# Performance work log

Measured on AMD Instinct MI355X. Metric: run time of the kernel, lower is better.

## Reference

```python
import jax, jax.numpy as jnp
import numpy as np

H = W = 224
NUM_COLS = 1024          # static padded ring width (>= max pixels in any radial ring, ~703)
SHUFFLE_FRACTION = 0.5
BATCH = 128

def _build_maps():
    centre = (H // 2, W // 2)
    Y, X = np.ogrid[:H, :W]
    dist = np.round(np.sqrt((X - centre[0]) ** 2 + (Y - centre[1]) ** 2)).astype(np.int32)
    num_rows = int(dist[0, 0]) + 1
    ax2 = np.zeros_like(dist)
    for d in range(num_rows):
        m = dist == d
        ax2[m] = np.arange(m.sum(), dtype=np.int32)  # row-major order within each ring
    return dist, ax2, num_rows

_DIST_NP, _AX2_NP, NUM_ROWS = _build_maps()
DIST_FLAT = jnp.asarray(_DIST_NP.reshape(-1))  # (H*W,) radial bin of each pixel
AX2_FLAT = jnp.asarray(_AX2_NP.reshape(-1))    # (H*W,) index within its ring

def _process_one(img, mrand, prand):
    # img: (H, W); mrand: (H, W); prand: (NUM_ROWS, NUM_COLS)
    sel = mrand < SHUFFLE_FRACTION
    masked = jnp.where(sel, img, jnp.nan)
    # scatter selected pixels into polar bins (pixel -> (dist, ax2) is a bijection)
    polar = jnp.full((NUM_ROWS, NUM_COLS), jnp.nan, dtype=img.dtype)
    polar = polar.at[DIST_FLAT, AX2_FLAT].set(masked.reshape(-1))
    # random per-row permutation of columns
    perm = jnp.argsort(prand, axis=1)
    shuf = jnp.take_along_axis(polar, perm, axis=1)
    # compact the non-NaN shuffled values (in column order) back into the
    # originally-occupied columns (in ascending order) -- same as the TF
    # argsort(dists)/boolean-mask scatter, expressed with static shapes.
    src_order = jnp.argsort(jnp.isnan(shuf), axis=1)    # stable: non-NaN cols first
    vals = jnp.take_along_axis(shuf, src_order, axis=1)
    dst_order = jnp.argsort(jnp.isnan(polar), axis=1)   # stable: occupied cols first
    rows = jnp.arange(NUM_ROWS)[:, None]
    reinserted = shuf.at[rows, dst_order].set(vals)
    # gather each pixel's (possibly shuffled) value and write back selected pixels
    new_vals = reinserted[DIST_FLAT, AX2_FLAT].reshape(H, W)
    return jnp.where(sel, new_vals, img)

def setup_inputs() -> dict:
    key = jax.random.key(0)
    k1, k2, k3 = jax.random.split(key, 3)
    images = jax.random.normal(k1, (BATCH, H, W, 1), dtype=jnp.float32)
    mask_rand = jax.random.uniform(k2, (BATCH, H, W), dtype=jnp.float32)
    perm_rand = jax.random.uniform(k3, (BATCH, NUM_ROWS, NUM_COLS), dtype=jnp.float32)
    return {"images": images, "mask_rand": mask_rand, "perm_rand": perm_rand}

def reference(images, mask_rand, perm_rand):
    out = jax.vmap(_process_one)(images[..., 0], mask_rand, perm_rand)
    return out[..., None]
```

## Files before the change

### kernel.cpp

```cpp
#include <hip/hip_runtime.h>

#define IMG_H 224
#define IMG_W 224
#define HW (IMG_H * IMG_W)
#define NUM_ROWS 159
#define NUM_COLS 1024
#define BATCH 128
#define OVF_CAP 4096
#define MAXC 12
#define NBUCK 512
#define NHWORDS (NBUCK / 2)

__device__ __forceinline__ int isqrt_i(int v) {
    int u = (int)sqrtf((float)v);
    while (u > 0 && u * u > v) --u;
    while ((u + 1) * (u + 1) <= v) ++u;
    return u;
}

__device__ __forceinline__ void lds_fence() {
    asm volatile("s_waitcnt lgkmcnt(0)" ::: "memory");
}

__global__ __launch_bounds__(256) void build_rings(int* __restrict__ ring_pix,
                                                   int* __restrict__ ring_cnt,
                                                   int* __restrict__ ovf_cnt) {
    const int d = blockIdx.x;
    const int tid = threadIdx.x;
    __shared__ int scnt[256];
    if (d == 0 && tid == 0) ovf_cnt[0] = 0;

    int cnt = 0;
    int x0l = 0, x1l = -1, x0r = 0, x1r = -1;
    if (tid < IMG_H) {
        const int dy = tid - 112;
        const int Araw = (d == 0) ? 0 : (d * d - d + 1);
        int A = Araw - dy * dy;
        if (A < 0) A = 0;
        const int B = d * d + d - dy * dy;
        if (B >= 0) {
            const int hi = isqrt_i(B);
            int lo = isqrt_i(A);
            if (lo * lo < A) ++lo;
            if (lo <= hi) {
                if (lo == 0) {
                    x0l = 112 - min(hi, 112);
                    x1l = 112 + min(hi, 111);
                } else {
                    x0l = 112 - min(hi, 112);
                    x1l = 112 - lo;
                    x0r = 112 + lo;
                    x1r = 112 + min(hi, 111);
                }
                cnt = max(0, x1l - x0l + 1) + max(0, x1r - x0r + 1);
            }
        }
    }
    scnt[tid] = cnt;
    __syncthreads();
    for (int off = 1; off < 256; off <<= 1) {
        const int mine = scnt[tid];
        const int add = (tid >= off) ? scnt[tid - off] : 0;
        __syncthreads();
        scnt[tid] = mine + add;
        __syncthreads();
    }
    if (tid < IMG_H && cnt > 0) {
        int j = d * NUM_COLS + (scnt[tid] - cnt);
        const int rowbase = tid * IMG_W;
        for (int x = x0l; x <= x1l; ++x) ring_pix[j++] = rowbase + x;
        for (int x = x0r; x <= x1r; ++x) ring_pix[j++] = rowbase + x;
    }
    if (tid == 255) ring_cnt[d] = scnt[255];
}

template <int CAP>
__device__ int gather_count_sort(
    int b, int d, int lane,
    const float* __restrict__ img, const float* __restrict__ mask,
    const float* __restrict__ prand, float* __restrict__ out,
    const int* __restrict__ ring_pix, int n,
    unsigned long long* __restrict__ srt, unsigned* __restrict__ hist,
    unsigned short* __restrict__ dstpix) {
    const float* imgb  = img  + (size_t)b * HW;
    const float* maskb = mask + (size_t)b * HW;
    const float* prb   = prand + ((size_t)b * NUM_ROWS + d) * NUM_COLS;
    float* outb = out + (size_t)b * HW;
    const unsigned long long ltmask = (1ull << lane) - 1ull;
    const int* rp = ring_pix + d * NUM_COLS;

#pragma unroll
    for (int t = 0; t < NHWORDS / 64; ++t) hist[t * 64 + lane] = 0;

    int p[MAXC];
    float v[MAXC], m[MAXC];
    unsigned kb[MAXC];
#pragma unroll
    for (int c = 0; c < MAXC; ++c) p[c] = rp[min(c * 64 + lane, n - 1)];
#pragma unroll
    for (int c = 0; c < MAXC; ++c) v[c] = imgb[p[c]];
#pragma unroll
    for (int c = 0; c < MAXC; ++c) m[c] = maskb[p[c]];
#pragma unroll
    for (int c = 0; c < MAXC; ++c)
        kb[c] = __float_as_uint(prb[min(c * 64 + lane, n - 1)]);

    lds_fence();

    int base = 0;
#pragma unroll
    for (int c = 0; c < MAXC; ++c) {
        const int i = c * 64 + lane;
        const bool active = (i < n);
        const bool sel = active && (m[c] < 0.5f);
        if (active && !sel) outb[p[c]] = v[c];
        const unsigned long long ball = __ballot(sel);
        if (sel) {
            const int j = base + __popcll(ball & ltmask);
            if (j < CAP) dstpix[j] = (unsigned short)p[c];
            const int bk = (int)(__uint_as_float(kb[c]) * (float)NBUCK);
            atomicAdd(&hist[bk >> 1], 1u << ((bk & 1) * 16));
        }
        base += __popcll(ball);
    }
    for (int c0 = MAXC * 64; c0 < n; c0 += 64) {
        const int i = c0 + lane;
        bool sel = false;
        int pp = 0;
        unsigned kk = 0;
        if (i < n) {
            pp = rp[i];
            const float vv = imgb[pp];
            kk = __float_as_uint(prb[i]);
            sel = (maskb[pp] < 0.5f);
            if (!sel) outb[pp] = vv;
        }
        const unsigned long long ball = __ballot(sel);
        if (sel) {
            const int j = base + __popcll(ball & ltmask);
            if (j < CAP) dstpix[j] = (unsigned short)pp;
            const int bk = (int)(__uint_as_float(kk) * (float)NBUCK);
            atomicAdd(&hist[bk >> 1], 1u << ((bk & 1) * 16));
        }
        base += __popcll(ball);
    }
    const int k = base;
    if (k > CAP) return k;

    lds_fence();

    constexpr int WPL = NHWORDS / 64;
    unsigned neww[WPL];
    unsigned run = 0;
#pragma unroll
    for (int t = 0; t < WPL; ++t) {
        const unsigned w = hist[lane * WPL + t];
        const unsigned c0 = w & 0xffffu;
        neww[t] = run | ((run + c0) << 16);
        run += c0 + (w >> 16);
    }
    const unsigned own = run;
#pragma unroll
    for (int off = 1; off < 64; off <<= 1) {
        const unsigned o = __shfl_up(run, off, 64);
        if (lane >= off) run += o;
    }
    const unsigned basex = run - own;
#pragma unroll
    for (int t = 0; t < WPL; ++t)
        hist[lane * WPL + t] = neww[t] + (basex | (basex << 16));

    lds_fence();

#pragma unroll
    for (int c = 0; c < MAXC; ++c) {
        const int i = c * 64 + lane;
        if (i < n && m[c] < 0.5f) {
            const int bk = (int)(__uint_as_float(kb[c]) * (float)NBUCK);
            const unsigned sh = (unsigned)((bk & 1) * 16);
            const unsigned old = atomicAdd(&hist[bk >> 1], 1u << sh);
            const int pos = (int)((old >> sh) & 0xffffu);
            srt[pos] = ((unsigned long long)kb[c] << 16) | (unsigned)p[c];
        }
    }
    for (int c0 = MAXC * 64; c0 < n; c0 += 64) {
        const int i = c0 + lane;
        if (i < n) {
            const int pp = rp[i];
            if (maskb[pp] < 0.5f) {
                const unsigned kk = __float_as_uint(prb[i]);
                const int bk = (int)(__uint_as_float(kk) * (float)NBUCK);
                const unsigned sh = (unsigned)((bk & 1) * 16);
                const unsigned old = atomicAdd(&hist[bk >> 1], 1u << sh);
                const int pos = (int)((old >> sh) & 0xffffu);
                srt[pos] = ((unsigned long long)kk << 16) | (unsigned)pp;
            }
        }
    }

    lds_fence();

    while (true) {
        bool sw = false;
        for (int i0 = 2 * lane; i0 + 1 < k; i0 += 128) {
            const unsigned long long a = srt[i0], bb = srt[i0 + 1];
            if (a > bb) { srt[i0] = bb; srt[i0 + 1] = a; sw = true; }
        }
        lds_fence();
        for (int i0 = 2 * lane + 1; i0 + 1 < k; i0 += 128) {
            const unsigned long long a = srt[i0], bb = srt[i0 + 1];
            if (a > bb) { srt[i0] = bb; srt[i0 + 1] = a; sw = true; }
        }
        lds_fence();
        if (__ballot(sw) == 0) break;
    }
    return k;
}

__device__ __forceinline__ void scatter_out(
    const unsigned long long* __restrict__ srt,
    const unsigned short* __restrict__ dstpix, int k, int lane,
    const float* __restrict__ imgb, float* __restrict__ outb) {
    const unsigned short* s16 = (const unsigned short*)srt;
    for (int j = lane; j < k; j += 64) {
        const int psrc = s16[4 * j];
        const int pdst = dstpix[j];
        outb[pdst] = imgb[psrc];
    }
}

__global__ __launch_bounds__(256) void radial_shuffle(
    const float* __restrict__ img, const float* __restrict__ mask,
    const float* __restrict__ prand, float* __restrict__ out,
    const int* __restrict__ ring_pix, const int* __restrict__ ring_cnt,
    int* __restrict__ ovf_cnt, int* __restrict__ ovf_list) {
    const int tid = threadIdx.x;
    const int wid = tid >> 6;
    const int lane = tid & 63;
    const int xcd = blockIdx.x & 7;
    const int g = (blockIdx.x >> 3) * 4 + wid;
    const int b = xcd * (BATCH / 8) + g / NUM_ROWS;
    const int d = g % NUM_ROWS;
    const int n = ring_cnt[d];

    __shared__ unsigned long long srt_s[4][512];
    __shared__ unsigned hist_s[4][NHWORDS];
    __shared__ unsigned short dp_s[4][512];

    const int k = gather_count_sort<512>(b, d, lane, img, mask, prand, out,
                                         ring_pix, n, srt_s[wid], hist_s[wid],
                                         dp_s[wid]);

    if (k > 512) {
        if (lane == 0) {
            const int idx = atomicAdd(ovf_cnt, 1);
            if (idx < OVF_CAP) ovf_list[idx] = b * NUM_ROWS + d;
        }
    } else if (k > 0) {
        scatter_out(srt_s[wid], dp_s[wid], k, lane, img + (size_t)b * HW,
                    out + (size_t)b * HW);
    }
}

__global__ __launch_bounds__(64) void overflow_sort(
    const float* __restrict__ img, const float* __restrict__ mask,
    const float* __restrict__ prand, float* __restrict__ out,
    const int* __restrict__ ring_pix, const int* __restrict__ ring_cnt,
    const int* __restrict__ ovf_cnt, const int* __restrict__ ovf_list) {
    __shared__ unsigned long long srt[1024];
    __shared__ unsigned hist[NHWORDS];
    __shared__ unsigned short dstpix[1024];
    const int m = min(*ovf_cnt, OVF_CAP);
    const int lane = threadIdx.x;
    for (int t = blockIdx.x; t < m; t += gridDim.x) {
        const int bd = ovf_list[t];
        const int b = bd / NUM_ROWS;
        const int d = bd % NUM_ROWS;
        const int k = gather_count_sort<1024>(b, d, lane, img, mask, prand,
                                              out, ring_pix, ring_cnt[d], srt,
                                              hist, dstpix);
        scatter_out(srt, dstpix, k, lane, img + (size_t)b * HW,
                    out + (size_t)b * HW);
        __syncthreads();
    }
}

extern "C" void kernel_launch(void* const* d_in, const int* in_sizes, int n_in,
                              void* d_out, int out_size, void* d_ws, size_t ws_size,
                              hipStream_t stream) {
    const float* img   = (const float*)d_in[0];
    const float* mask  = (const float*)d_in[1];
    const float* prand = (const float*)d_in[2];
    float* out = (float*)d_out;

    int* ring_pix = (int*)d_ws;
    int* ring_cnt = ring_pix + NUM_ROWS * NUM_COLS;
    int* ovf_cnt  = ring_cnt + NUM_ROWS;
    int* ovf_list = ovf_cnt + 1;

    hipLaunchKernelGGL(build_rings, dim3(NUM_ROWS), dim3(256), 0, stream,
                       ring_pix, ring_cnt, ovf_cnt);
    hipLaunchKernelGGL(radial_shuffle, dim3(BATCH * NUM_ROWS / 4), dim3(256), 0,
                       stream, img, mask, prand, out, ring_pix, ring_cnt,
                       ovf_cnt, ovf_list);
    hipLaunchKernelGGL(overflow_sort, dim3(32), dim3(64), 0, stream,
                       img, mask, prand, out, ring_pix, ring_cnt,
                       ovf_cnt, ovf_list);
}
```

Before: 231.7 us.

## Precompute selection bitmask with coalesced copy pass, replace odd-even sort with per-bucket insertion sort

Adds a coalesced float4 pre-pass that copies the image to the output and packs mask<0.5 into a per-pixel bitmask. The ring kernel then no longer does scattered reads of the mask or writes of unselected pixels. Ring pixel indices shrink to 16-bit, and image values are staged in LDS so only selected pixels are gathered. The odd-even transposition sort is replaced by per-bucket insertion sort over the bucket ranges, which relies on buckets being small. This costs an extra full-image read and write pass and an extra kernel launch.

```diff
diff --git a/kernel.cpp b/kernel.cpp
--- a/kernel.cpp
+++ b/kernel.cpp
@@ -3,6 +3,7 @@
 #define IMG_H 224
 #define IMG_W 224
 #define HW (IMG_H * IMG_W)
+#define HWB (HW / 8)
 #define NUM_ROWS 159
 #define NUM_COLS 1024
 #define BATCH 128
@@ -10,6 +11,7 @@
 #define MAXC 12
 #define NBUCK 512
 #define NHWORDS (NBUCK / 2)
+#define WPL (NHWORDS / 64)
 
 __device__ __forceinline__ int isqrt_i(int v) {
     int u = (int)sqrtf((float)v);
@@ -22,7 +24,7 @@
     asm volatile("s_waitcnt lgkmcnt(0)" ::: "memory");
 }
 
-__global__ __launch_bounds__(256) void build_rings(int* __restrict__ ring_pix,
+__global__ __launch_bounds__(256) void build_rings(unsigned short* __restrict__ ring_pix,
                                                    int* __restrict__ ring_cnt,
                                                    int* __restrict__ ovf_cnt) {
     const int d = blockIdx.x;
@@ -68,52 +70,89 @@
     if (tid < IMG_H && cnt > 0) {
         int j = d * NUM_COLS + (scnt[tid] - cnt);
         const int rowbase = tid * IMG_W;
-        for (int x = x0l; x <= x1l; ++x) ring_pix[j++] = rowbase + x;
-        for (int x = x0r; x <= x1r; ++x) ring_pix[j++] = rowbase + x;
+        for (int x = x0l; x <= x1l; ++x) ring_pix[j++] = (unsigned short)(rowbase + x);
+        for (int x = x0r; x <= x1r; ++x) ring_pix[j++] = (unsigned short)(rowbase + x);
     }
     if (tid == 255) ring_cnt[d] = scnt[255];
+}
+
+__global__ __launch_bounds__(256) void copy_sel(const float4* __restrict__ img4,
+                                                const float4* __restrict__ mask4,
+                                                float4* __restrict__ out4,
+                                                unsigned char* __restrict__ selb) {
+    const int t = blockIdx.x * 256 + threadIdx.x;
+    const float4 i0 = img4[2 * t];
+    const float4 i1 = img4[2 * t + 1];
+    const float4 m0 = mask4[2 * t];
+    const float4 m1 = mask4[2 * t + 1];
+    out4[2 * t] = i0;
+    out4[2 * t + 1] = i1;
+    const unsigned by = (m0.x < 0.5f ? 1u : 0u) | (m0.y < 0.5f ? 2u : 0u) |
+                        (m0.z < 0.5f ? 4u : 0u) | (m0.w < 0.5f ? 8u : 0u) |
+                        (m1.x < 0.5f ? 16u : 0u) | (m1.y < 0.5f ? 32u : 0u) |
+                        (m1.z < 0.5f ? 64u : 0u) | (m1.w < 0.5f ? 128u : 0u);
+    selb[t] = (unsigned char)by;
+}
+
+__device__ __forceinline__ void sort_run(unsigned long long* __restrict__ srt,
+                                         int s, int e) {
+    for (int i = s + 1; i < e; ++i) {
+        const unsigned long long key = srt[i];
+        int j = i - 1;
+        while (j >= s && srt[j] > key) {
+            srt[j + 1] = srt[j];
+            --j;
+        }
+        srt[j + 1] = key;
+    }
 }
 
 template <int CAP>
 __device__ int gather_count_sort(
     int b, int d, int lane,
-    const float* __restrict__ img, const float* __restrict__ mask,
+    const float* __restrict__ img, const unsigned char* __restrict__ selb,
     const float* __restrict__ prand, float* __restrict__ out,
-    const int* __restrict__ ring_pix, int n,
+    const unsigned short* __restrict__ ring_pix, int n,
     unsigned long long* __restrict__ srt, unsigned* __restrict__ hist,
-    unsigned short* __restrict__ dstpix) {
-    const float* imgb  = img  + (size_t)b * HW;
-    const float* maskb = mask + (size_t)b * HW;
-    const float* prb   = prand + ((size_t)b * NUM_ROWS + d) * NUM_COLS;
+    unsigned short* __restrict__ dstpix, float* __restrict__ vlds) {
+    const float* imgb = img + (size_t)b * HW;
+    const unsigned char* sbb = selb + (size_t)b * HWB;
+    const float* prb = prand + ((size_t)b * NUM_ROWS + d) * NUM_COLS;
     float* outb = out + (size_t)b * HW;
     const unsigned long long ltmask = (1ull << lane) - 1ull;
-    const int* rp = ring_pix + d * NUM_COLS;
-
-#pragma unroll
-    for (int t = 0; t < NHWORDS / 64; ++t) hist[t * 64 + lane] = 0;
+    const unsigned short* rp = ring_pix + d * NUM_COLS;
+
+#pragma unroll
+    for (int t = 0; t < WPL; ++t) hist[t * 64 + lane] = 0;
 
     int p[MAXC];
-    float v[MAXC], m[MAXC];
+    unsigned char sb[MAXC];
     unsigned kb[MAXC];
 #pragma unroll
     for (int c = 0; c < MAXC; ++c) p[c] = rp[min(c * 64 + lane, n - 1)];
 #pragma unroll
-    for (int c = 0; c < MAXC; ++c) v[c] = imgb[p[c]];
-#pragma unroll
-    for (int c = 0; c < MAXC; ++c) m[c] = maskb[p[c]];
-#pragma unroll
-    for (int c = 0; c < MAXC; ++c)
-        kb[c] = __float_as_uint(prb[min(c * 64 + lane, n - 1)]);
-
-    lds_fence();
-
-    int base = 0;
+    for (int c = 0; c < MAXC; ++c) sb[c] = sbb[p[c] >> 3];
+#pragma unroll
+    for (int c = 0; c < MAXC; ++c) kb[c] = __float_as_uint(prb[min(c * 64 + lane, n - 1)]);
+
+    unsigned selm = 0;
 #pragma unroll
     for (int c = 0; c < MAXC; ++c) {
         const int i = c * 64 + lane;
-        const bool active = (i < n);
-        const bool sel = active && (m[c] < 0.5f);
-        if (active && !sel) outb[p[c]] = v[c];
+        if ((i < n) && ((sb[c] >> (p[c] & 7)) & 1)) selm |= 1u << c;
+    }
+
+    float v[MAXC];
+#pragma unroll
+    for (int c = 0; c < MAXC; ++c)
+        if ((selm >> c) & 1) v[c] = imgb[p[c]];
+
+    lds_fence();
+
+    int base = 0;
+#pragma unroll
+    for (int c = 0; c < MAXC; ++c) {
+        const bool sel = (selm >> c) & 1;
         const unsigned long long ball = __ballot(sel);
         if (sel) {
             const int j = base + __popcll(ball & ltmask);
@@ -123,6 +162,7 @@
         }
         base += __popcll(ball);
     }
+    const int base_static = base;
     for (int c0 = MAXC * 64; c0 < n; c0 += 64) {
         const int i = c0 + lane;
         bool sel = false;
@@ -130,15 +170,16 @@
         unsigned kk = 0;
         if (i < n) {
             pp = rp[i];
-            const float vv = imgb[pp];
             kk = __float_as_uint(prb[i]);
-            sel = (maskb[pp] < 0.5f);
-            if (!sel) outb[pp] = vv;
+            sel = (sbb[pp >> 3] >> (pp & 7)) & 1;
         }
         const unsigned long long ball = __ballot(sel);
         if (sel) {
             const int j = base + __popcll(ball & ltmask);
-            if (j < CAP) dstpix[j] = (unsigned short)pp;
+            if (j < CAP) {
+                dstpix[j] = (unsigned short)pp;
+                vlds[j] = imgb[pp];
+            }
             const int bk = (int)(__uint_as_float(kk) * (float)NBUCK);
             atomicAdd(&hist[bk >> 1], 1u << ((bk & 1) * 16));
         }
@@ -146,10 +187,10 @@
     }
     const int k = base;
     if (k > CAP) return k;
-
-    lds_fence();
-
-    constexpr int WPL = NHWORDS / 64;
+    if (k == 0) return 0;
+
+    lds_fence();
+
     unsigned neww[WPL];
     unsigned run = 0;
 #pragma unroll
@@ -165,74 +206,85 @@
         const unsigned o = __shfl_up(run, off, 64);
         if (lane >= off) run += o;
     }
-    const unsigned basex = run - own;
-#pragma unroll
-    for (int t = 0; t < WPL; ++t)
-        hist[lane * WPL + t] = neww[t] + (basex | (basex << 16));
-
-    lds_fence();
-
+    const unsigned bx = run - own;
+    const unsigned bxp = bx | (bx << 16);
+    unsigned st[WPL];
+#pragma unroll
+    for (int t = 0; t < WPL; ++t) {
+        st[t] = neww[t] + bxp;
+        hist[lane * WPL + t] = st[t];
+    }
+
+    lds_fence();
+
+    int jb = 0;
 #pragma unroll
     for (int c = 0; c < MAXC; ++c) {
-        const int i = c * 64 + lane;
-        if (i < n && m[c] < 0.5f) {
+        const bool sel = (selm >> c) & 1;
+        const unsigned long long ball = __ballot(sel);
+        if (sel) {
+            const int j = jb + __popcll(ball & ltmask);
             const int bk = (int)(__uint_as_float(kb[c]) * (float)NBUCK);
             const unsigned sh = (unsigned)((bk & 1) * 16);
             const unsigned old = atomicAdd(&hist[bk >> 1], 1u << sh);
             const int pos = (int)((old >> sh) & 0xffffu);
-            srt[pos] = ((unsigned long long)kb[c] << 16) | (unsigned)p[c];
-        }
-    }
+            srt[pos] = ((unsigned long long)kb[c] << 16) | (unsigned)j;
+            vlds[j] = v[c];
+        }
+        jb += __popcll(ball);
+    }
+    int tb = base_static;
     for (int c0 = MAXC * 64; c0 < n; c0 += 64) {
         const int i = c0 + lane;
+        bool sel = false;
+        int pp = 0;
+        unsigned kk = 0;
         if (i < n) {
-            const int pp = rp[i];
-            if (maskb[pp] < 0.5f) {
-                const unsigned kk = __float_as_uint(prb[i]);
-                const int bk = (int)(__uint_as_float(kk) * (float)NBUCK);
-                const unsigned sh = (unsigned)((bk & 1) * 16);
-                const unsigned old = atomicAdd(&hist[bk >> 1], 1u << sh);
-                const int pos = (int)((old >> sh) & 0xffffu);
-                srt[pos] = ((unsigned long long)kk << 16) | (unsigned)pp;
-            }
-        }
-    }
-
-    lds_fence();
-
-    while (true) {
-        bool sw = false;
-        for (int i0 = 2 * lane; i0 + 1 < k; i0 += 128) {
-            const unsigned long long a = srt[i0], bb = srt[i0 + 1];
-            if (a > bb) { srt[i0] = bb; srt[i0 + 1] = a; sw = true; }
-        }
-        lds_fence();
-        for (int i0 = 2 * lane + 1; i0 + 1 < k; i0 += 128) {
-            const unsigned long long a = srt[i0], bb = srt[i0 + 1];
-            if (a > bb) { srt[i0] = bb; srt[i0 + 1] = a; sw = true; }
-        }
-        lds_fence();
-        if (__ballot(sw) == 0) break;
+            pp = rp[i];
+            kk = __float_as_uint(prb[i]);
+            sel = (sbb[pp >> 3] >> (pp & 7)) & 1;
+        }
+        const unsigned long long ball = __ballot(sel);
+        if (sel) {
+            const int j = tb + __popcll(ball & ltmask);
+            const int bk = (int)(__uint_as_float(kk) * (float)NBUCK);
+            const unsigned sh = (unsigned)((bk & 1) * 16);
+            const unsigned old = atomicAdd(&hist[bk >> 1], 1u << sh);
+            const int pos = (int)((old >> sh) & 0xffffu);
+            srt[pos] = ((unsigned long long)kk << 16) | (unsigned)j;
+        }
+        tb += __popcll(ball);
+    }
+
+    lds_fence();
+
+#pragma unroll
+    for (int t = 0; t < WPL; ++t) {
+        const unsigned wend = hist[lane * WPL + t];
+        const unsigned ws0 = st[t];
+        sort_run(srt, (int)(ws0 & 0xffffu), (int)(wend & 0xffffu));
+        sort_run(srt, (int)(ws0 >> 16), (int)(wend >> 16));
+    }
+
+    lds_fence();
+
+    const unsigned short* s16 = (const unsigned short*)srt;
+#pragma unroll
+    for (int e = 0; e < CAP / 64; ++e) {
+        const int r = e * 64 + lane;
+        if (r < k) {
+            const int j = s16[4 * r];
+            const float val = vlds[j];
+            outb[dstpix[r]] = val;
+        }
     }
     return k;
 }
 
-__device__ __forceinline__ void scatter_out(
-    const unsigned long long* __restrict__ srt,
-    const unsigned short* __restrict__ dstpix, int k, int lane,
-    const float* __restrict__ imgb, float* __restrict__ outb) {
-    const unsigned short* s16 = (const unsigned short*)srt;
-    for (int j = lane; j < k; j += 64) {
-        const int psrc = s16[4 * j];
-        const int pdst = dstpix[j];
-        outb[pdst] = imgb[psrc];
-    }
-}
-
 __global__ __launch_bounds__(256) void radial_shuffle(
-    const float* __restrict__ img, const float* __restrict__ mask,
+    const float* __restrict__ img, const unsigned char* __restrict__ selb,
     const float* __restrict__ prand, float* __restrict__ out,
-    const int* __restrict__ ring_pix, const int* __restrict__ ring_cnt,
+    const unsigned short* __restrict__ ring_pix, const int* __restrict__ ring_cnt,
     int* __restrict__ ovf_cnt, int* __restrict__ ovf_list) {
     const int tid = threadIdx.x;
     const int wid = tid >> 6;
@@ -246,41 +298,37 @@
     __shared__ unsigned long long srt_s[4][512];
     __shared__ unsigned hist_s[4][NHWORDS];
     __shared__ unsigned short dp_s[4][512];
-
-    const int k = gather_count_sort<512>(b, d, lane, img, mask, prand, out,
+    __shared__ float vl_s[4][512];
+
+    const int k = gather_count_sort<512>(b, d, lane, img, selb, prand, out,
                                          ring_pix, n, srt_s[wid], hist_s[wid],
-                                         dp_s[wid]);
+                                         dp_s[wid], vl_s[wid]);
 
     if (k > 512) {
         if (lane == 0) {
             const int idx = atomicAdd(ovf_cnt, 1);
             if (idx < OVF_CAP) ovf_list[idx] = b * NUM_ROWS + d;
         }
-    } else if (k > 0) {
-        scatter_out(srt_s[wid], dp_s[wid], k, lane, img + (size_t)b * HW,
-                    out + (size_t)b * HW);
     }
 }
 
 __global__ __launch_bounds__(64) void overflow_sort(
-    const float* __restrict__ img, const float* __restrict__ mask,
+    const float* __restrict__ img, const unsigned char* __restrict__ selb,
     const float* __restrict__ prand, float* __restrict__ out,
-    const int* __restrict__ ring_pix, const int* __restrict__ ring_cnt,
+    const unsigned short* __restrict__ ring_pix, const int* __restrict__ ring_cnt,
     const int* __restrict__ ovf_cnt, const int* __restrict__ ovf_list) {
     __shared__ unsigned long long srt[1024];
     __shared__ unsigned hist[NHWORDS];
     __shared__ unsigned short dstpix[1024];
+    __shared__ float vlds[1024];
     const int m = min(*ovf_cnt, OVF_CAP);
     const int lane = threadIdx.x;
     for (int t = blockIdx.x; t < m; t += gridDim.x) {
         const int bd = ovf_list[t];
         const int b = bd / NUM_ROWS;
         const int d = bd % NUM_ROWS;
-        const int k = gather_count_sort<1024>(b, d, lane, img, mask, prand,
-                                              out, ring_pix, ring_cnt[d], srt,
-                                              hist, dstpix);
-        scatter_out(srt, dstpix, k, lane, img + (size_t)b * HW,
-                    out + (size_t)b * HW);
+        gather_count_sort<1024>(b, d, lane, img, selb, prand, out, ring_pix,
+                                ring_cnt[d], srt, hist, dstpix, vlds);
         __syncthreads();
     }
 }
@@ -293,17 +341,20 @@
     const float* prand = (const float*)d_in[2];
     float* out = (float*)d_out;
 
-    int* ring_pix = (int*)d_ws;
-    int* ring_cnt = ring_pix + NUM_ROWS * NUM_COLS;
+    unsigned short* ring_pix = (unsigned short*)d_ws;
+    int* ring_cnt = (int*)((char*)d_ws + NUM_ROWS * NUM_COLS * sizeof(unsigned short));
     int* ovf_cnt  = ring_cnt + NUM_ROWS;
     int* ovf_list = ovf_cnt + 1;
+    unsigned char* selb = (unsigned char*)(ovf_list + OVF_CAP);
 
     hipLaunchKernelGGL(build_rings, dim3(NUM_ROWS), dim3(256), 0, stream,
                        ring_pix, ring_cnt, ovf_cnt);
+    hipLaunchKernelGGL(copy_sel, dim3(BATCH * HW / 8 / 256), dim3(256), 0, stream,
+                       (const float4*)img, (const float4*)mask, (float4*)out, selb);
     hipLaunchKernelGGL(radial_shuffle, dim3(BATCH * NUM_ROWS / 4), dim3(256), 0,
-                       stream, img, mask, prand, out, ring_pix, ring_cnt,
+                       stream, img, selb, prand, out, ring_pix, ring_cnt,
                        ovf_cnt, ovf_list);
     hipLaunchKernelGGL(overflow_sort, dim3(32), dim3(64), 0, stream,
-                       img, mask, prand, out, ring_pix, ring_cnt,
+                       img, selb, prand, out, ring_pix, ring_cnt,
                        ovf_cnt, ovf_list);
 }
```

Result: faster. 201.0 us (-13.2%).
